# Optimization experiments

Hardware: AMD Instinct MI355X
Metric: run time of the kernel (lower is better)

## Reference

```python
import jax, jax.numpy as jnp
import numpy as np

S, B, I, H = 512, 8192, 3, 5  # seq, batch, input_size, hidden_size


def _uniform(key, shape, bound):
    return jax.random.uniform(key, shape, jnp.float32, -bound, bound)


def setup_inputs() -> dict:
    key = jax.random.key(0)
    ks = jax.random.split(key, 17)
    bound = 1.0 / np.sqrt(H)
    inp = {"x": jax.random.normal(ks[0], (S, B, I), jnp.float32)}
    # layer 0: in=I ; layer 1: in=2H (concat of both directions). Suffix 'r' = reverse direction.
    specs = [
        ("l0", I), ("l0r", I), ("l1", 2 * H), ("l1r", 2 * H),
    ]
    ki = 1
    for name, din in specs:
        inp[f"w_ih_{name}"] = _uniform(ks[ki], (4 * H, din), bound); ki += 1
        inp[f"w_hh_{name}"] = _uniform(ks[ki], (4 * H, H), bound); ki += 1
        inp[f"b_ih_{name}"] = _uniform(ks[ki], (4 * H,), bound); ki += 1
        inp[f"b_hh_{name}"] = _uniform(ks[ki], (4 * H,), bound); ki += 1
    return inp


def _lstm_dir(x, w_ih, w_hh, b_ih, b_hh, reverse):
    """Single-direction LSTM over x [S,B,Din] -> (hs [S,B,H], h_T [B,H], c_T [B,H])."""
    xs = x[::-1] if reverse else x
    # Precompute input contributions for all timesteps in one big matmul.
    gx = jnp.einsum('sbi,gi->sbg', xs, w_ih) + b_ih + b_hh  # [S,B,4H]
    h0 = jnp.zeros((x.shape[1], H), x.dtype)
    c0 = jnp.zeros((x.shape[1], H), x.dtype)

    def step(carry, g):
        h, c = carry
        g = g + h @ w_hh.T  # [B,4H]
        i, f, gg, o = jnp.split(g, 4, axis=-1)  # PyTorch gate order: i,f,g,o
        i = jax.nn.sigmoid(i)
        f = jax.nn.sigmoid(f)
        gg = jnp.tanh(gg)
        o = jax.nn.sigmoid(o)
        c = f * c + i * gg
        h = o * jnp.tanh(c)
        return (h, c), h

    (hT, cT), hs = jax.lax.scan(step, (h0, c0), gx)
    if reverse:
        hs = hs[::-1]
    return hs, hT, cT


def reference(x,
              w_ih_l0, w_hh_l0, b_ih_l0, b_hh_l0,
              w_ih_l0r, w_hh_l0r, b_ih_l0r, b_hh_l0r,
              w_ih_l1, w_hh_l1, b_ih_l1, b_hh_l1,
              w_ih_l1r, w_hh_l1r, b_ih_l1r, b_hh_l1r):
    # Layer 0 (bidirectional)
    hs0f, h0f, c0f = _lstm_dir(x, w_ih_l0, w_hh_l0, b_ih_l0, b_hh_l0, False)
    hs0b, h0b, c0b = _lstm_dir(x, w_ih_l0r, w_hh_l0r, b_ih_l0r, b_hh_l0r, True)
    out0 = jnp.concatenate([hs0f, hs0b], axis=-1)  # [S,B,2H]
    # Layer 1 (bidirectional) consumes concat of both directions
    hs1f, h1f, c1f = _lstm_dir(out0, w_ih_l1, w_hh_l1, b_ih_l1, b_hh_l1, False)
    hs1b, h1b, c1b = _lstm_dir(out0, w_ih_l1r, w_hh_l1r, b_ih_l1r, b_hh_l1r, True)
    output = jnp.concatenate([hs1f, hs1b], axis=-1)  # [S,B,2H]
    # PyTorch h_n/c_n layout: [num_layers*num_directions, B, H] ordered (l0 fwd, l0 bwd, l1 fwd, l1 bwd)
    h_n = jnp.stack([h0f, h0b, h1f, h1b], axis=0)
    c_n = jnp.stack([c0f, c0b, c1f, c1b], axis=0)
    return output, h_n, c_n
```

## Files before the change

### kernel.cpp

```cpp
#include <hip/hip_runtime.h>


constexpr int S_ = 512;
constexpr int B_ = 8192;
constexpr int NROW = 16384;

constexpr int GD1  = 2048;
constexpr int TL   = 240;
constexpr int GSTR = GD1 * 64;

constexpr float L2E  = 1.4426950408889634f;
constexpr float T2E  = 2.8853900817779268f;
constexpr float IT2E = 0.34657359027997264f;

typedef _Float16 v2h __attribute__((ext_vector_type(2)));

__device__ __forceinline__ float dot2h(v2h a, v2h b, float c) {
#if __has_builtin(__builtin_amdgcn_fdot2)
    return __builtin_amdgcn_fdot2(a, b, c, false);
#else
    return fmaf((float)a[0], (float)b[0], fmaf((float)a[1], (float)b[1], c));
#endif
}

__device__ __forceinline__ float rcp_(float x) { return __builtin_amdgcn_rcpf(x); }

__device__ __forceinline__ float exp2_(float x) {
#if __has_builtin(__builtin_amdgcn_exp2f)
    return __builtin_amdgcn_exp2f(x);
#else
    return exp2f(x);
#endif
}

__device__ __forceinline__ void sbar() { __builtin_amdgcn_sched_barrier(0); }

__device__ __forceinline__ float bperm(int bidx, float v) {
    return __int_as_float(__builtin_amdgcn_ds_bpermute(bidx, __float_as_int(v)));
}

__device__ __forceinline__ unsigned pkh(float a, float b) {
    auto t = __builtin_amdgcn_cvt_pkrtz(a, b);
    unsigned q; __builtin_memcpy(&q, &t, 4); return q;
}

__device__ __forceinline__ unsigned short f2h(float x) {
    _Float16 h = (_Float16)x;
    unsigned short s; __builtin_memcpy(&s, &h, 2); return s;
}

__device__ __forceinline__ float h2f(unsigned short s) {
    _Float16 h; __builtin_memcpy(&h, &s, 2); return (float)h;
}

__global__ __launch_bounds__(64) __attribute__((amdgpu_waves_per_eu(1, 2)))
void lstm_layer0(
    const float* __restrict__ x,
    const float* __restrict__ wih_f, const float* __restrict__ whh_f,
    const float* __restrict__ bih_f, const float* __restrict__ bhh_f,
    const float* __restrict__ wih_r, const float* __restrict__ whh_r,
    const float* __restrict__ bih_r, const float* __restrict__ bhh_r,
    unsigned short* __restrict__ ws,
    float* __restrict__ outbase)
{
    const int l64 = threadIdx.x & 63;
    int r = l64 / 5; r = (r > 11) ? 11 : r;
    const int u   = l64 - r * 5;
    const int uc  = (u < 5) ? u : 4;
    const int gid = blockIdx.x * 12 + r;
    const bool valid = gid < NROW;
    const int dir = (gid >> 13) & 1;
    const int b   = gid & 8191;
    const bool stw = valid && (u < 3);
    const bool st  = valid && (u < 5);

    int bidx[5];
#pragma unroll
    for (int k = 0; k < 5; k++) bidx[k] = (r * 5 + k) * 4;

    const float* __restrict__ wih = dir ? wih_r : wih_f;
    const float* __restrict__ whh = dir ? whh_r : whh_f;
    const float* __restrict__ bih = dir ? bih_r : bih_f;
    const float* __restrict__ bhh = dir ? bhh_r : bhh_f;

    const int rows[4] = {uc, 5 + uc, 10 + uc, 15 + uc};
    const float scl[4] = {-L2E, -L2E, T2E, -L2E};
    float WX[4][3], WH[4][5], BS[4];
#pragma unroll
    for (int gi = 0; gi < 4; gi++) {
        const int rr = rows[gi]; const float sc = scl[gi];
#pragma unroll
        for (int i = 0; i < 3; i++) WX[gi][i] = wih[rr * 3 + i] * sc;
#pragma unroll
        for (int k = 0; k < 5; k++) WH[gi][k] = whh[rr * 5 + k] * sc;
        BS[gi] = (bih[rr] + bhh[rr]) * sc;
    }

    float h[5] = {0.f, 0.f, 0.f, 0.f, 0.f};
    float cp = 0.f, hu_last = 0.f;

    const int t0 = dir ? (S_ - 1) : 0;
    const float* xp = x + ((size_t)t0 * B_ + b) * 3;
    unsigned short* wp = ws + (size_t)dir * ((size_t)S_ * B_ * 6)
                            + ((size_t)t0 * B_ + b) * 6;
    const ptrdiff_t xst = dir ? -(ptrdiff_t)3 * B_ : (ptrdiff_t)3 * B_;
    const ptrdiff_t wst = dir ? -(ptrdiff_t)6 * B_ : (ptrdiff_t)6 * B_;

    auto step = [&](const float (&xin)[3], unsigned short* wpp) {
        float a0 = BS[0], a1 = BS[1], a2 = BS[2], a3 = BS[3];
#pragma unroll
        for (int i = 0; i < 3; i++) {
            a0 = fmaf(WX[0][i], xin[i], a0);
            a1 = fmaf(WX[1][i], xin[i], a1);
            a2 = fmaf(WX[2][i], xin[i], a2);
            a3 = fmaf(WX[3][i], xin[i], a3);
        }
#pragma unroll
        for (int k = 0; k < 5; k++) {
            a0 = fmaf(WH[0][k], h[k], a0);
            a1 = fmaf(WH[1][k], h[k], a1);
            a2 = fmaf(WH[2][k], h[k], a2);
            a3 = fmaf(WH[3][k], h[k], a3);
        }
        const float ig = rcp_(1.0f + exp2_(a0));
        const float fg = rcp_(1.0f + exp2_(a1));
        const float g2 = fmaf(-2.0f * T2E, rcp_(1.0f + exp2_(a2)), T2E);
        const float og = rcp_(1.0f + exp2_(a3));
        cp = fmaf(fg, cp, ig * g2);
        const float th = fmaf(-2.0f, rcp_(1.0f + exp2_(cp)), 1.0f);
        const float hu = og * th;
        hu_last = hu;
#pragma unroll
        for (int k = 0; k < 5; k++) h[k] = bperm(bidx[k], hu);
        const unsigned q0 = pkh(h[0], h[1]);
        const unsigned q1 = pkh(h[2], h[3]);
        const unsigned q2 = pkh(h[4], 0.0f);
        unsigned qs = q0;
        qs = (u == 1) ? q1 : qs;
        qs = (u == 2) ? q2 : qs;
        if (stw) ((unsigned*)wpp)[u] = qs;
    };

    auto ld = [&](float (&buf)[3]) {
        __builtin_memcpy(&buf[0], xp, 12);
        xp += xst;
        sbar();
    };

    float x0[3], x1[3], x2[3], x3[3], x4[3], x5[3], x6[3], x7[3];
    ld(x0); ld(x1); ld(x2); ld(x3); ld(x4); ld(x5); ld(x6); ld(x7);

#pragma unroll 1
    for (int s = 0; s < S_ - 8; s += 8) {
        step(x0, wp); wp += wst; ld(x0);
        step(x1, wp); wp += wst; ld(x1);
        step(x2, wp); wp += wst; ld(x2);
        step(x3, wp); wp += wst; ld(x3);
        step(x4, wp); wp += wst; ld(x4);
        step(x5, wp); wp += wst; ld(x5);
        step(x6, wp); wp += wst; ld(x6);
        step(x7, wp); wp += wst; ld(x7);
    }
    step(x0, wp); wp += wst;
    step(x1, wp); wp += wst;
    step(x2, wp); wp += wst;
    step(x3, wp); wp += wst;
    step(x4, wp); wp += wst;
    step(x5, wp); wp += wst;
    step(x6, wp); wp += wst;
    step(x7, wp);

    const size_t OUTE = (size_t)S_ * B_ * 10;
    float* hn = outbase + OUTE + ((size_t)dir * B_ + b) * 5;
    float* cn = hn + (size_t)4 * B_ * 5;
    if (st) { hn[uc] = hu_last; cn[uc] = cp * IT2E; }
}

__global__ __launch_bounds__(64) __attribute__((amdgpu_waves_per_eu(2, 4)))
void lstm_layer1(
    const unsigned short* __restrict__ ws,
    const float* __restrict__ wih_f, const float* __restrict__ whh_f,
    const float* __restrict__ bih_f, const float* __restrict__ bhh_f,
    const float* __restrict__ wih_r, const float* __restrict__ whh_r,
    const float* __restrict__ bih_r, const float* __restrict__ bhh_r,
    float* __restrict__ outbase,
    unsigned short* __restrict__ gtemp)
{
    __shared__ unsigned short lt[TL * 40];

    const int l64 = threadIdx.x & 63;
    const int r  = l64 >> 3;
    const int u  = l64 & 7;
    const int uc = (u < 5) ? u : 4;
    const int rm  = r & 3;
    const int dir = r >> 2;
    const int b   = blockIdx.x * 4 + rm;
    const bool st = (u < 5);
    const int dir5 = dir * 5;
    const int pr  = dir ? (r - 4) : (r + 4);
    const int psL = pr * 5 + uc;
    const int psG = pr * 8 + uc;

    int bidx[5];
#pragma unroll
    for (int k = 0; k < 5; k++) bidx[k] = (r * 8 + k) * 4;

    const float* __restrict__ wih = dir ? wih_r : wih_f;
    const float* __restrict__ whh = dir ? whh_r : whh_f;
    const float* __restrict__ bih = dir ? bih_r : bih_f;
    const float* __restrict__ bhh = dir ? bhh_r : bhh_f;

    const int rows[4] = {uc, 5 + uc, 10 + uc, 15 + uc};
    const float scl[4] = {-L2E, -L2E, T2E, -L2E};
    v2h WX[4][6];
    float WH[4][5], BS[4];
#pragma unroll
    for (int gi = 0; gi < 4; gi++) {
        const int rr = rows[gi]; const float sc = scl[gi];
#pragma unroll
        for (int p = 0; p < 6; p++) {
            const int i0 = (p < 3) ? 2 * p : 2 * p - 1;
            const bool pad = (p == 2) || (p == 5);
            const float w0 = wih[rr * 10 + i0] * sc;
            const float w1 = pad ? 0.f : wih[rr * 10 + i0 + 1] * sc;
            WX[gi][p] = (v2h){(_Float16)w0, (_Float16)w1};
        }
#pragma unroll
        for (int k = 0; k < 5; k++) WH[gi][k] = whh[rr * 5 + k] * sc;
        BS[gi] = (bih[rr] + bhh[rr]) * sc;
    }

    float h[5] = {0.f, 0.f, 0.f, 0.f, 0.f};
    float cp = 0.f, hu_last = 0.f;

    const int t0 = dir ? (S_ - 1) : 0;
    const unsigned short* rpf = ws + ((size_t)t0 * B_ + b) * 6;
    const unsigned short* rpb = rpf + (size_t)S_ * B_ * 6;
    float* op = outbase + ((size_t)(dir ? 255 : 256) * B_ + b) * 10;
    const ptrdiff_t rst = dir ? -(ptrdiff_t)6 * B_ : (ptrdiff_t)6 * B_;
    const ptrdiff_t ost = dir ? -(ptrdiff_t)10 * B_ : (ptrdiff_t)10 * B_;

    unsigned short* gw = gtemp + (size_t)blockIdx.x * 64 + l64;
    const unsigned short* gr = gtemp + (size_t)15 * GSTR
                                     + (size_t)blockIdx.x * 64 + psG;

    auto core = [&](const v2h (&xin)[6]) -> float {
        float a0 = BS[0], a1 = BS[1], a2 = BS[2], a3 = BS[3];
#pragma unroll
        for (int p = 0; p < 6; p++) {
            a0 = dot2h(xin[p], WX[0][p], a0);
            a1 = dot2h(xin[p], WX[1][p], a1);
            a2 = dot2h(xin[p], WX[2][p], a2);
            a3 = dot2h(xin[p], WX[3][p], a3);
        }
#pragma unroll
        for (int k = 0; k < 5; k++) {
            a0 = fmaf(WH[0][k], h[k], a0);
            a1 = fmaf(WH[1][k], h[k], a1);
            a2 = fmaf(WH[2][k], h[k], a2);
            a3 = fmaf(WH[3][k], h[k], a3);
        }
        const float ig = rcp_(1.0f + exp2_(a0));
        const float fg = rcp_(1.0f + exp2_(a1));
        const float g2 = fmaf(-2.0f * T2E, rcp_(1.0f + exp2_(a2)), T2E);
        const float og = rcp_(1.0f + exp2_(a3));
        cp = fmaf(fg, cp, ig * g2);
        const float th = fmaf(-2.0f, rcp_(1.0f + exp2_(cp)), 1.0f);
        const float hu = og * th;
        hu_last = hu;
        return hu;
    };

    auto bcast = [&](float hu) {
#pragma unroll
        for (int k = 0; k < 5; k++) h[k] = bperm(bidx[k], hu);
    };

    auto step1L = [&](const v2h (&xin)[6], int t) {
        const float hu = core(xin);
        if (st) lt[t * 40 + r * 5 + u] = f2h(hu);
        bcast(hu);
    };
    auto step1G = [&](const v2h (&xin)[6]) {
        const float hu = core(xin);
        *gw = f2h(hu);
        gw += GSTR;
        bcast(hu);
    };
    auto step2G = [&](const v2h (&xin)[6], unsigned short pvs, float* opp) {
        const float pv = h2f(pvs);
        const float hu = core(xin);
        if (st) { opp[dir5 + u] = hu; opp[5 - dir5 + u] = pv; }
        bcast(hu);
    };
    auto step2L = [&](const v2h (&xin)[6], int t, float* opp) {
        const float pv = h2f(lt[(511 - t) * 40 + psL]);
        const float hu = core(xin);
        if (st) { opp[dir5 + u] = hu; opp[5 - dir5 + u] = pv; }
        bcast(hu);
    };

    auto ld = [&](v2h (&buf)[6]) {
        __builtin_memcpy(&buf[0], rpf, 12);
        __builtin_memcpy(&buf[3], rpb, 12);
        rpf += rst; rpb += rst;
        sbar();
    };

    v2h x0[6], x1[6], x2[6], x3[6];
    ld(x0); ld(x1); ld(x2); ld(x3);

#pragma unroll 1
    for (int t = 0; t < TL; t += 4) {
        step1L(x0, t + 0); ld(x0);
        step1L(x1, t + 1); ld(x1);
        step1L(x2, t + 2); ld(x2);
        step1L(x3, t + 3); ld(x3);
    }
#pragma unroll 1
    for (int t = TL; t < 256; t += 4) {
        step1G(x0); ld(x0);
        step1G(x1); ld(x1);
        step1G(x2); ld(x2);
        step1G(x3); ld(x3);
    }
    asm volatile("s_waitcnt vmcnt(0)" ::: "memory");
    unsigned short pva = *gr; gr -= GSTR;
    unsigned short pvb = *gr; gr -= GSTR;
    unsigned short pvc = *gr; gr -= GSTR;
    unsigned short pvd = *gr; gr -= GSTR;
#pragma unroll 1
    for (int t = 256; t < 272; t += 4) {
        step2G(x0, pva, op); op += ost; pva = *gr; gr -= GSTR; ld(x0);
        step2G(x1, pvb, op); op += ost; pvb = *gr; gr -= GSTR; ld(x1);
        step2G(x2, pvc, op); op += ost; pvc = *gr; gr -= GSTR; ld(x2);
        step2G(x3, pvd, op); op += ost; pvd = *gr; gr -= GSTR; ld(x3);
    }
#pragma unroll 1
    for (int t = 272; t < 508; t += 4) {
        step2L(x0, t + 0, op); op += ost; ld(x0);
        step2L(x1, t + 1, op); op += ost; ld(x1);
        step2L(x2, t + 2, op); op += ost; ld(x2);
        step2L(x3, t + 3, op); op += ost; ld(x3);
    }
    step2L(x0, 508, op); op += ost;
    step2L(x1, 509, op); op += ost;
    step2L(x2, 510, op); op += ost;
    step2L(x3, 511, op);

    const size_t OUTE = (size_t)S_ * B_ * 10;
    float* hn = outbase + OUTE + ((size_t)(2 + dir) * B_ + b) * 5;
    float* cn = hn + (size_t)4 * B_ * 5;
    if (st) { hn[u] = hu_last; cn[u] = cp * IT2E; }
}

extern "C" void kernel_launch(void* const* d_in, const int* in_sizes, int n_in,
                              void* d_out, int out_size, void* d_ws, size_t ws_size,
                              hipStream_t stream) {
    const float* x       = (const float*)d_in[0];
    const float* wih_l0  = (const float*)d_in[1];
    const float* whh_l0  = (const float*)d_in[2];
    const float* bih_l0  = (const float*)d_in[3];
    const float* bhh_l0  = (const float*)d_in[4];
    const float* wih_l0r = (const float*)d_in[5];
    const float* whh_l0r = (const float*)d_in[6];
    const float* bih_l0r = (const float*)d_in[7];
    const float* bhh_l0r = (const float*)d_in[8];
    const float* wih_l1  = (const float*)d_in[9];
    const float* whh_l1  = (const float*)d_in[10];
    const float* bih_l1  = (const float*)d_in[11];
    const float* bhh_l1  = (const float*)d_in[12];
    const float* wih_l1r = (const float*)d_in[13];
    const float* whh_l1r = (const float*)d_in[14];
    const float* bih_l1r = (const float*)d_in[15];
    const float* bhh_l1r = (const float*)d_in[16];

    float* out = (float*)d_out;
    unsigned short* ws = (unsigned short*)d_ws;
    unsigned short* gtemp = ws + (size_t)2 * S_ * B_ * 6 + (size_t)4 * GSTR;

    dim3 grid0(1366), block(64);
    lstm_layer0<<<grid0, block, 0, stream>>>(x,
        wih_l0, whh_l0, bih_l0, bhh_l0,
        wih_l0r, whh_l0r, bih_l0r, bhh_l0r,
        ws, out);
    dim3 grid1(GD1);
    lstm_layer1<<<grid1, block, 0, stream>>>(ws,
        wih_l1, whh_l1, bih_l1, bhh_l1,
        wih_l1r, whh_l1r, bih_l1r, bhh_l1r,
        out, gtemp);
}
```

Measured before the change: 327.5 us.

## Deepen layer-1 input prefetch, use ds_swizzle broadcast, swizzle block-to-batch mapping

Layer-1 LSTM kernel changes in several ways. The input prefetch ring grows from 4 to 8 buffers, and each step computes the input dot products before reissuing the load, so the recurrent dependency chain is shorter. The ds_bpermute hidden-state broadcast becomes ds_swizzle with fixed patterns, which drops the per-lane index registers. Blocks are remapped to batch rows with a stride-256 interleave, and the 16 global spill values are loaded up front instead of through a rolling pointer. The gtemp workspace offset also moves. The extra buffers raise register pressure, and the swizzle pattern and the remap must still match the original lane and batch layout.

```diff
diff --git a/kernel.cpp b/kernel.cpp
--- a/kernel.cpp
+++ b/kernel.cpp
@@ -189,21 +189,19 @@
     __shared__ unsigned short lt[TL * 40];
 
     const int l64 = threadIdx.x & 63;
+    const int bid = (int)blockIdx.x;
+    const int bsw = (bid & 7) * 256 + (bid >> 3);
     const int r  = l64 >> 3;
     const int u  = l64 & 7;
     const int uc = (u < 5) ? u : 4;
     const int rm  = r & 3;
     const int dir = r >> 2;
-    const int b   = blockIdx.x * 4 + rm;
+    const int b   = bsw * 4 + rm;
     const bool st = (u < 5);
     const int dir5 = dir * 5;
     const int pr  = dir ? (r - 4) : (r + 4);
     const int psL = pr * 5 + uc;
     const int psG = pr * 8 + uc;
-
-    int bidx[5];
-#pragma unroll
-    for (int k = 0; k < 5; k++) bidx[k] = (r * 8 + k) * 4;
 
     const float* __restrict__ wih = dir ? wih_r : wih_f;
     const float* __restrict__ whh = dir ? whh_r : whh_f;
@@ -240,30 +238,35 @@
     const ptrdiff_t rst = dir ? -(ptrdiff_t)6 * B_ : (ptrdiff_t)6 * B_;
     const ptrdiff_t ost = dir ? -(ptrdiff_t)10 * B_ : (ptrdiff_t)10 * B_;
 
-    unsigned short* gw = gtemp + (size_t)blockIdx.x * 64 + l64;
-    const unsigned short* gr = gtemp + (size_t)15 * GSTR
-                                     + (size_t)blockIdx.x * 64 + psG;
-
-    auto core = [&](const v2h (&xin)[6]) -> float {
-        float a0 = BS[0], a1 = BS[1], a2 = BS[2], a3 = BS[3];
+    unsigned short* gw = gtemp + (size_t)bid * 64 + l64;
+
+    struct A4 { float a0, a1, a2, a3; };
+
+    auto dots = [&](const v2h (&xin)[6]) -> A4 {
+        A4 v;
+        v.a0 = BS[0]; v.a1 = BS[1]; v.a2 = BS[2]; v.a3 = BS[3];
 #pragma unroll
         for (int p = 0; p < 6; p++) {
-            a0 = dot2h(xin[p], WX[0][p], a0);
-            a1 = dot2h(xin[p], WX[1][p], a1);
-            a2 = dot2h(xin[p], WX[2][p], a2);
-            a3 = dot2h(xin[p], WX[3][p], a3);
+            v.a0 = dot2h(xin[p], WX[0][p], v.a0);
+            v.a1 = dot2h(xin[p], WX[1][p], v.a1);
+            v.a2 = dot2h(xin[p], WX[2][p], v.a2);
+            v.a3 = dot2h(xin[p], WX[3][p], v.a3);
         }
+        return v;
+    };
+
+    auto cell = [&](A4 v) -> float {
 #pragma unroll
         for (int k = 0; k < 5; k++) {
-            a0 = fmaf(WH[0][k], h[k], a0);
-            a1 = fmaf(WH[1][k], h[k], a1);
-            a2 = fmaf(WH[2][k], h[k], a2);
-            a3 = fmaf(WH[3][k], h[k], a3);
+            v.a0 = fmaf(WH[0][k], h[k], v.a0);
+            v.a1 = fmaf(WH[1][k], h[k], v.a1);
+            v.a2 = fmaf(WH[2][k], h[k], v.a2);
+            v.a3 = fmaf(WH[3][k], h[k], v.a3);
         }
-        const float ig = rcp_(1.0f + exp2_(a0));
-        const float fg = rcp_(1.0f + exp2_(a1));
-        const float g2 = fmaf(-2.0f * T2E, rcp_(1.0f + exp2_(a2)), T2E);
-        const float og = rcp_(1.0f + exp2_(a3));
+        const float ig = rcp_(1.0f + exp2_(v.a0));
+        const float fg = rcp_(1.0f + exp2_(v.a1));
+        const float g2 = fmaf(-2.0f * T2E, rcp_(1.0f + exp2_(v.a2)), T2E);
+        const float og = rcp_(1.0f + exp2_(v.a3));
         cp = fmaf(fg, cp, ig * g2);
         const float th = fmaf(-2.0f, rcp_(1.0f + exp2_(cp)), 1.0f);
         const float hu = og * th;
@@ -272,32 +275,12 @@
     };
 
     auto bcast = [&](float hu) {
-#pragma unroll
-        for (int k = 0; k < 5; k++) h[k] = bperm(bidx[k], hu);
-    };
-
-    auto step1L = [&](const v2h (&xin)[6], int t) {
-        const float hu = core(xin);
-        if (st) lt[t * 40 + r * 5 + u] = f2h(hu);
-        bcast(hu);
-    };
-    auto step1G = [&](const v2h (&xin)[6]) {
-        const float hu = core(xin);
-        *gw = f2h(hu);
-        gw += GSTR;
-        bcast(hu);
-    };
-    auto step2G = [&](const v2h (&xin)[6], unsigned short pvs, float* opp) {
-        const float pv = h2f(pvs);
-        const float hu = core(xin);
-        if (st) { opp[dir5 + u] = hu; opp[5 - dir5 + u] = pv; }
-        bcast(hu);
-    };
-    auto step2L = [&](const v2h (&xin)[6], int t, float* opp) {
-        const float pv = h2f(lt[(511 - t) * 40 + psL]);
-        const float hu = core(xin);
-        if (st) { opp[dir5 + u] = hu; opp[5 - dir5 + u] = pv; }
-        bcast(hu);
+        const int v = __float_as_int(hu);
+        h[0] = __int_as_float(__builtin_amdgcn_ds_swizzle(v, 0x18 | (0 << 5)));
+        h[1] = __int_as_float(__builtin_amdgcn_ds_swizzle(v, 0x18 | (1 << 5)));
+        h[2] = __int_as_float(__builtin_amdgcn_ds_swizzle(v, 0x18 | (2 << 5)));
+        h[3] = __int_as_float(__builtin_amdgcn_ds_swizzle(v, 0x18 | (3 << 5)));
+        h[4] = __int_as_float(__builtin_amdgcn_ds_swizzle(v, 0x18 | (4 << 5)));
     };
 
     auto ld = [&](v2h (&buf)[6]) {
@@ -307,46 +290,80 @@
         sbar();
     };
 
-    v2h x0[6], x1[6], x2[6], x3[6];
-    ld(x0); ld(x1); ld(x2); ld(x3);
+    auto s1L = [&](v2h (&xb)[6], int t) {
+        A4 a = dots(xb); ld(xb);
+        const float hu = cell(a); bcast(hu);
+        if (st) lt[t * 40 + r * 5 + u] = f2h(hu);
+    };
+    auto s1G = [&](v2h (&xb)[6]) {
+        A4 a = dots(xb); ld(xb);
+        const float hu = cell(a); bcast(hu);
+        *gw = f2h(hu); gw += GSTR;
+    };
+    auto s2G = [&](v2h (&xb)[6], unsigned short pvs) {
+        A4 a = dots(xb); ld(xb);
+        const float pv = h2f(pvs);
+        const float hu = cell(a); bcast(hu);
+        if (st) { op[dir5 + u] = hu; op[5 - dir5 + u] = pv; }
+        op += ost;
+    };
+    auto s2L = [&](v2h (&xb)[6], int t) {
+        const float pv = h2f(lt[(511 - t) * 40 + psL]);
+        A4 a = dots(xb); ld(xb);
+        const float hu = cell(a); bcast(hu);
+        if (st) { op[dir5 + u] = hu; op[5 - dir5 + u] = pv; }
+        op += ost;
+    };
+    auto s2Ln = [&](v2h (&xb)[6], int t) {
+        const float pv = h2f(lt[(511 - t) * 40 + psL]);
+        A4 a = dots(xb);
+        const float hu = cell(a); bcast(hu);
+        if (st) { op[dir5 + u] = hu; op[5 - dir5 + u] = pv; }
+        op += ost;
+    };
+
+    v2h x0[6], x1[6], x2[6], x3[6], x4[6], x5[6], x6[6], x7[6];
+    ld(x0); ld(x1); ld(x2); ld(x3); ld(x4); ld(x5); ld(x6); ld(x7);
 
 #pragma unroll 1
-    for (int t = 0; t < TL; t += 4) {
-        step1L(x0, t + 0); ld(x0);
-        step1L(x1, t + 1); ld(x1);
-        step1L(x2, t + 2); ld(x2);
-        step1L(x3, t + 3); ld(x3);
+    for (int t = 0; t < TL; t += 8) {
+        s1L(x0, t + 0); s1L(x1, t + 1); s1L(x2, t + 2); s1L(x3, t + 3);
+        s1L(x4, t + 4); s1L(x5, t + 5); s1L(x6, t + 6); s1L(x7, t + 7);
     }
 #pragma unroll 1
-    for (int t = TL; t < 256; t += 4) {
-        step1G(x0); ld(x0);
-        step1G(x1); ld(x1);
-        step1G(x2); ld(x2);
-        step1G(x3); ld(x3);
+    for (int t = TL; t < 256; t += 8) {
+        s1G(x0); s1G(x1); s1G(x2); s1G(x3);
+        s1G(x4); s1G(x5); s1G(x6); s1G(x7);
     }
     asm volatile("s_waitcnt vmcnt(0)" ::: "memory");
-    unsigned short pva = *gr; gr -= GSTR;
-    unsigned short pvb = *gr; gr -= GSTR;
-    unsigned short pvc = *gr; gr -= GSTR;
-    unsigned short pvd = *gr; gr -= GSTR;
+    const unsigned short* g0 = gtemp + (size_t)bid * 64 + psG;
+    const unsigned short q15 = g0[(size_t)15 * GSTR];
+    const unsigned short q14 = g0[(size_t)14 * GSTR];
+    const unsigned short q13 = g0[(size_t)13 * GSTR];
+    const unsigned short q12 = g0[(size_t)12 * GSTR];
+    const unsigned short q11 = g0[(size_t)11 * GSTR];
+    const unsigned short q10 = g0[(size_t)10 * GSTR];
+    const unsigned short q9  = g0[(size_t)9  * GSTR];
+    const unsigned short q8  = g0[(size_t)8  * GSTR];
+    const unsigned short q7  = g0[(size_t)7  * GSTR];
+    const unsigned short q6  = g0[(size_t)6  * GSTR];
+    const unsigned short q5  = g0[(size_t)5  * GSTR];
+    const unsigned short q4  = g0[(size_t)4  * GSTR];
+    const unsigned short q3  = g0[(size_t)3  * GSTR];
+    const unsigned short q2  = g0[(size_t)2  * GSTR];
+    const unsigned short q1  = g0[(size_t)1  * GSTR];
+    const unsigned short q0  = g0[0];
+    s2G(x0, q15); s2G(x1, q14); s2G(x2, q13); s2G(x3, q12);
+    s2G(x4, q11); s2G(x5, q10); s2G(x6, q9);  s2G(x7, q8);
+    s2G(x0, q7);  s2G(x1, q6);  s2G(x2, q5);  s2G(x3, q4);
+    s2G(x4, q3);  s2G(x5, q2);  s2G(x6, q1);  s2G(x7, q0);
 #pragma unroll 1
-    for (int t = 256; t < 272; t += 4) {
-        step2G(x0, pva, op); op += ost; pva = *gr; gr -= GSTR; ld(x0);
-        step2G(x1, pvb, op); op += ost; pvb = *gr; gr -= GSTR; ld(x1);
-        step2G(x2, pvc, op); op += ost; pvc = *gr; gr -= GSTR; ld(x2);
-        step2G(x3, pvd, op); op += ost; pvd = *gr; gr -= GSTR; ld(x3);
-    }
-#pragma unroll 1
-    for (int t = 272; t < 508; t += 4) {
-        step2L(x0, t + 0, op); op += ost; ld(x0);
-        step2L(x1, t + 1, op); op += ost; ld(x1);
-        step2L(x2, t + 2, op); op += ost; ld(x2);
-        step2L(x3, t + 3, op); op += ost; ld(x3);
-    }
-    step2L(x0, 508, op); op += ost;
-    step2L(x1, 509, op); op += ost;
-    step2L(x2, 510, op); op += ost;
-    step2L(x3, 511, op);
+    for (int t = 272; t < 504; t += 8) {
+        s2L(x0, t + 0); s2L(x1, t + 1); s2L(x2, t + 2); s2L(x3, t + 3);
+        s2L(x4, t + 4); s2L(x5, t + 5); s2L(x6, t + 6); s2L(x7, t + 7);
+    }
+    s2Ln(x0, 504); s2Ln(x1, 505); s2Ln(x2, 506); s2Ln(x3, 507);
+    s2Ln(x4, 508); s2Ln(x5, 509); s2Ln(x6, 510); s2Ln(x7, 511);
 
     const size_t OUTE = (size_t)S_ * B_ * 10;
     float* hn = outbase + OUTE + ((size_t)(2 + dir) * B_ + b) * 5;
@@ -377,7 +394,7 @@
 
     float* out = (float*)d_out;
     unsigned short* ws = (unsigned short*)d_ws;
-    unsigned short* gtemp = ws + (size_t)2 * S_ * B_ * 6 + (size_t)4 * GSTR;
+    unsigned short* gtemp = ws + (size_t)2 * S_ * B_ * 6;
 
     dim3 grid0(1366), block(64);
     lstm_layer0<<<grid0, block, 0, stream>>>(x,
```

New measurement: 308.9 us. 1.06x faster.
